# Optimization experiments

Measured on AMD Instinct MI355X. Metric: run time of the kernel, lower is better.

## Reference

```python
import jax, jax.numpy as jnp
import numpy as np

B, T, D, E, K = 4, 4096, 2048, 64, 2


def setup_inputs() -> dict:
    key = jax.random.key(0)
    k1, k2 = jax.random.split(key)
    x = jax.random.normal(k1, (B, T, D), dtype=jnp.float32)
    # nn.Linear(token_dim, n_experts, bias=False) weight: [E, D]
    gate_w = jax.random.normal(k2, (E, D), dtype=jnp.float32) * (1.0 / np.sqrt(D))
    return {"x": x, "gate_w": gate_w}


def reference(x, gate_w):
    # logits = x @ gate_w.T : [B, T, E]
    logits = jnp.einsum("btd,ed->bte", x, gate_w)
    scores, indices = jax.lax.top_k(logits, K)  # [B, T, K] each
    weights = jax.nn.softmax(scores, axis=-1)
    return weights, indices
```

## Files before the change

### kernel.cpp

```cpp
#include <hip/hip_runtime.h>
#include <math.h>


#define NTOK 16384
#define DDIM 2048
#define NEXP 64
#define TBLK 64
#define KC   32
#define NKG  4
#define NCH  16

typedef __attribute__((ext_vector_type(8))) _Float16 f16x8;
typedef __attribute__((ext_vector_type(4))) float f32x4;

#define XF_OFF 0
#define WF_OFF 98304

__device__ static inline void gload_lds16(const void* gsrc, void* ldst) {
    __builtin_amdgcn_global_load_lds(
        (const __attribute__((address_space(1))) void*)gsrc,
        (__attribute__((address_space(3))) void*)ldst, 16, 0, 0);
}

__device__ static inline void split2h(float x, _Float16& h, _Float16& m) {
    h = (_Float16)x;
    float r = x - (float)h;
    m = (_Float16)r;
}

__global__ __launch_bounds__(512, 1) void moe_fused_kernel(
    const float* __restrict__ x,
    const float* __restrict__ gw,
    float* __restrict__ out)
{
    extern __shared__ char smem[];
    float4* XF = (float4*)(smem + XF_OFF);
    float4* WF = (float4*)(smem + WF_OFF);
    float*  red = (float*)smem;

    const int tid  = threadIdx.x;
    const int lane = tid & 63;
    const int w    = tid >> 6;
    const int kg   = w >> 1;
    const int tq   = w & 1;
    const int T0   = blockIdx.x * TBLK;

    const int fr  = lane & 15;
    const int fg  = lane >> 4;
    const int akey = fr & 7;

    f32x4 acc[2][4];
#pragma unroll
    for (int mi = 0; mi < 2; ++mi)
#pragma unroll
        for (int n = 0; n < 4; ++n) acc[mi][n] = (f32x4){0.f, 0.f, 0.f, 0.f};

#define XSTAGE(ch, buf)                                                       \
    {                                                                         \
        _Pragma("unroll")                                                     \
        for (int k = 0; k < 4; ++k) {                                         \
            const int u = tid + k * 512;                                      \
            const int s = u >> 9;                                             \
            const int r = (u >> 3) & 63;                                      \
            const int c = (u & 7) ^ (r & 7);                                  \
            gload_lds16(x + (size_t)(T0 + r) * DDIM + ((ch) * NKG + s) * KC + c * 4, \
                        &XF[(buf) * 2048 + u]);                               \
        }                                                                     \
    }
#define WSTAGE(ch, buf)                                                       \
    {                                                                         \
        _Pragma("unroll")                                                     \
        for (int k = 0; k < 4; ++k) {                                         \
            const int u = tid + k * 512;                                      \
            const int s = u >> 9;                                             \
            const int e = (u >> 3) & 63;                                      \
            const int c = (u & 7) ^ (e & 7);                                  \
            gload_lds16(gw + (size_t)e * DDIM + ((ch) * NKG + s) * KC + c * 4,\
                        &WF[(buf) * 2048 + u]);                               \
        }                                                                     \
    }
#define WAIT4 asm volatile("s_waitcnt vmcnt(4)" ::: "memory")
#define WAIT0 asm volatile("s_waitcnt vmcnt(0)" ::: "memory")
#define BAR   __builtin_amdgcn_s_barrier()

    XSTAGE(0, 0); WSTAGE(0, 0); XSTAGE(1, 1);
    WAIT4; BAR;

    for (int ch = 0; ch < NCH; ++ch) {
        const int xb = ch % 3;
        const int wb = ch & 1;
        if (ch + 1 < NCH) WSTAGE(ch + 1, (ch + 1) & 1);
        if (ch + 2 < NCH) XSTAGE(ch + 2, (ch + 2) % 3);

        const float4* Xc = &XF[xb * 2048 + kg * 512];
        f16x8 ah[2], am[2];
#pragma unroll
        for (int mi = 0; mi < 2; ++mi) {
            const int arow = (tq * 32 + mi * 16 + fr) * 8;
            float4 a0 = Xc[arow + ((fg * 2 + 0) ^ akey)];
            float4 a1 = Xc[arow + ((fg * 2 + 1) ^ akey)];
            float xf8[8] = {a0.x, a0.y, a0.z, a0.w, a1.x, a1.y, a1.z, a1.w};
#pragma unroll
            for (int j = 0; j < 8; ++j) {
                _Float16 hj, mj;
                split2h(xf8[j], hj, mj);
                ah[mi][j] = hj; am[mi][j] = mj;
            }
        }

        const float4* Wc = &WF[wb * 2048 + kg * 512];
#pragma unroll
        for (int n = 0; n < 4; ++n) {
            const int brow = (n * 16 + fr) * 8;
            float4 b0 = Wc[brow + ((fg * 2 + 0) ^ akey)];
            float4 b1 = Wc[brow + ((fg * 2 + 1) ^ akey)];
            float wf8[8] = {b0.x, b0.y, b0.z, b0.w, b1.x, b1.y, b1.z, b1.w};
            f16x8 bh, bm;
#pragma unroll
            for (int j = 0; j < 8; ++j) {
                _Float16 hj, mj;
                split2h(wf8[j], hj, mj);
                bh[j] = hj; bm[j] = mj;
            }
#pragma unroll
            for (int mi = 0; mi < 2; ++mi) {
                acc[mi][n] = __builtin_amdgcn_mfma_f32_16x16x32_f16(am[mi], bm, acc[mi][n], 0, 0, 0);
                acc[mi][n] = __builtin_amdgcn_mfma_f32_16x16x32_f16(am[mi], bh, acc[mi][n], 0, 0, 0);
                acc[mi][n] = __builtin_amdgcn_mfma_f32_16x16x32_f16(ah[mi], bm, acc[mi][n], 0, 0, 0);
                acc[mi][n] = __builtin_amdgcn_mfma_f32_16x16x32_f16(ah[mi], bh, acc[mi][n], 0, 0, 0);
            }
        }

        if (ch + 2 < NCH)      { WAIT4; BAR; }
        else if (ch + 1 < NCH) { WAIT0; BAR; }
        else                   { BAR; }
    }
#undef XSTAGE
#undef WSTAGE
#undef WAIT4
#undef WAIT0
#undef BAR

#pragma unroll
    for (int mi = 0; mi < 2; ++mi)
#pragma unroll
        for (int n = 0; n < 4; ++n)
#pragma unroll
            for (int j = 0; j < 4; ++j) {
                const int e = n * 16 + fr;
                const int t = tq * 32 + mi * 16 + fg * 4 + j;
                red[kg * 4160 + e * 65 + t] = acc[mi][n][j];
            }
    __syncthreads();

#pragma unroll
    for (int k = 0; k < 8; ++k) {
        const int q = tid + k * 512;
        const int e = q >> 6;
        const int t = q & 63;
        float s = red[0 * 4160 + e * 65 + t];
#pragma unroll
        for (int sl = 1; sl < NKG; ++sl)
            s += red[sl * 4160 + e * 65 + t];
        red[e * 65 + t] = s;
    }
    __syncthreads();

    if (tid < TBLK) {
        const int t = tid;
        float m1 = -INFINITY, m2 = -INFINITY;
        int i1 = 0, i2 = 0;
        for (int e = 0; e < NEXP; ++e) {
            float v = red[e * 65 + t];
            if (v > m1) {
                m2 = m1; i2 = i1;
                m1 = v;  i1 = e;
            } else if (v > m2) {
                m2 = v;  i2 = e;
            }
        }
        float e2 = expf(m2 - m1);
        float denom = 1.f + e2;
        const int gt = T0 + t;
        out[gt * 2 + 0] = 1.f / denom;
        out[gt * 2 + 1] = e2 / denom;
        out[NTOK * 2 + gt * 2 + 0] = (float)i1;
        out[NTOK * 2 + gt * 2 + 1] = (float)i2;
    }
}

extern "C" void kernel_launch(void* const* d_in, const int* in_sizes, int n_in,
                              void* d_out, int out_size, void* d_ws, size_t ws_size,
                              hipStream_t stream) {
    const float* x  = (const float*)d_in[0];
    const float* gw = (const float*)d_in[1];
    float* out = (float*)d_out;
    (void)d_ws; (void)ws_size;

    moe_fused_kernel<<<dim3(NTOK / TBLK), dim3(512), 163840, stream>>>(
        x, gw, out);
}
```

Baseline: 41.29 us.

## Shrink token tile to 32 with 256-thread blocks for two blocks per CU

Halves the token tile per block (64 to 32), halves the K-split groups and thread count, and cuts LDS per block so two blocks can fit per CU. The grid doubles to 512 blocks, which improves wave coverage across CUs and lets one block's loads overlap another's compute. The cost is that the gate weight matrix is streamed from L2 twice as often per token, and each block has less MFMA work between barriers.

```diff
diff --git a/kernel.cpp b/kernel.cpp
--- a/kernel.cpp
+++ b/kernel.cpp
@@ -5,16 +5,16 @@
 #define NTOK 16384
 #define DDIM 2048
 #define NEXP 64
-#define TBLK 64
+#define TBLK 32
 #define KC   32
-#define NKG  4
-#define NCH  16
+#define NKG  2
+#define NCH  32
 
 typedef __attribute__((ext_vector_type(8))) _Float16 f16x8;
 typedef __attribute__((ext_vector_type(4))) float f32x4;
 
 #define XF_OFF 0
-#define WF_OFF 98304
+#define WF_OFF 24576
 
 __device__ static inline void gload_lds16(const void* gsrc, void* ldst) {
     __builtin_amdgcn_global_load_lds(
@@ -28,7 +28,7 @@
     m = (_Float16)r;
 }
 
-__global__ __launch_bounds__(512, 1) void moe_fused_kernel(
+__global__ __launch_bounds__(256, 2) void moe_fused_kernel(
     const float* __restrict__ x,
     const float* __restrict__ gw,
     float* __restrict__ out)
@@ -49,42 +49,40 @@
     const int fg  = lane >> 4;
     const int akey = fr & 7;
 
-    f32x4 acc[2][4];
+    f32x4 acc[4];
 #pragma unroll
-    for (int mi = 0; mi < 2; ++mi)
-#pragma unroll
-        for (int n = 0; n < 4; ++n) acc[mi][n] = (f32x4){0.f, 0.f, 0.f, 0.f};
+    for (int n = 0; n < 4; ++n) acc[n] = (f32x4){0.f, 0.f, 0.f, 0.f};
 
 #define XSTAGE(ch, buf)                                                       \
     {                                                                         \
         _Pragma("unroll")                                                     \
-        for (int k = 0; k < 4; ++k) {                                         \
-            const int u = tid + k * 512;                                      \
-            const int s = u >> 9;                                             \
-            const int r = (u >> 3) & 63;                                      \
+        for (int k = 0; k < 2; ++k) {                                         \
+            const int u = tid + k * 256;                                      \
+            const int s = u >> 8;                                             \
+            const int r = (u >> 3) & 31;                                      \
             const int c = (u & 7) ^ (r & 7);                                  \
             gload_lds16(x + (size_t)(T0 + r) * DDIM + ((ch) * NKG + s) * KC + c * 4, \
-                        &XF[(buf) * 2048 + u]);                               \
+                        &XF[(buf) * 512 + u]);                                \
         }                                                                     \
     }
 #define WSTAGE(ch, buf)                                                       \
     {                                                                         \
         _Pragma("unroll")                                                     \
         for (int k = 0; k < 4; ++k) {                                         \
-            const int u = tid + k * 512;                                      \
+            const int u = tid + k * 256;                                      \
             const int s = u >> 9;                                             \
             const int e = (u >> 3) & 63;                                      \
             const int c = (u & 7) ^ (e & 7);                                  \
             gload_lds16(gw + (size_t)e * DDIM + ((ch) * NKG + s) * KC + c * 4,\
-                        &WF[(buf) * 2048 + u]);                               \
+                        &WF[(buf) * 1024 + u]);                               \
         }                                                                     \
     }
-#define WAIT4 asm volatile("s_waitcnt vmcnt(4)" ::: "memory")
+#define WAIT2 asm volatile("s_waitcnt vmcnt(2)" ::: "memory")
 #define WAIT0 asm volatile("s_waitcnt vmcnt(0)" ::: "memory")
 #define BAR   __builtin_amdgcn_s_barrier()
 
     XSTAGE(0, 0); WSTAGE(0, 0); XSTAGE(1, 1);
-    WAIT4; BAR;
+    WAIT2; BAR;
 
     for (int ch = 0; ch < NCH; ++ch) {
         const int xb = ch % 3;
@@ -92,11 +90,10 @@
         if (ch + 1 < NCH) WSTAGE(ch + 1, (ch + 1) & 1);
         if (ch + 2 < NCH) XSTAGE(ch + 2, (ch + 2) % 3);
 
-        const float4* Xc = &XF[xb * 2048 + kg * 512];
-        f16x8 ah[2], am[2];
-#pragma unroll
-        for (int mi = 0; mi < 2; ++mi) {
-            const int arow = (tq * 32 + mi * 16 + fr) * 8;
+        const float4* Xc = &XF[xb * 512 + kg * 256];
+        f16x8 ah, am;
+        {
+            const int arow = (tq * 16 + fr) * 8;
             float4 a0 = Xc[arow + ((fg * 2 + 0) ^ akey)];
             float4 a1 = Xc[arow + ((fg * 2 + 1) ^ akey)];
             float xf8[8] = {a0.x, a0.y, a0.z, a0.w, a1.x, a1.y, a1.z, a1.w};
@@ -104,11 +101,11 @@
             for (int j = 0; j < 8; ++j) {
                 _Float16 hj, mj;
                 split2h(xf8[j], hj, mj);
-                ah[mi][j] = hj; am[mi][j] = mj;
+                ah[j] = hj; am[j] = mj;
             }
         }
 
-        const float4* Wc = &WF[wb * 2048 + kg * 512];
+        const float4* Wc = &WF[wb * 1024 + kg * 512];
 #pragma unroll
         for (int n = 0; n < 4; ++n) {
             const int brow = (n * 16 + fr) * 8;
@@ -122,47 +119,38 @@
                 split2h(wf8[j], hj, mj);
                 bh[j] = hj; bm[j] = mj;
             }
-#pragma unroll
-            for (int mi = 0; mi < 2; ++mi) {
-                acc[mi][n] = __builtin_amdgcn_mfma_f32_16x16x32_f16(am[mi], bm, acc[mi][n], 0, 0, 0);
-                acc[mi][n] = __builtin_amdgcn_mfma_f32_16x16x32_f16(am[mi], bh, acc[mi][n], 0, 0, 0);
-                acc[mi][n] = __builtin_amdgcn_mfma_f32_16x16x32_f16(ah[mi], bm, acc[mi][n], 0, 0, 0);
-                acc[mi][n] = __builtin_amdgcn_mfma_f32_16x16x32_f16(ah[mi], bh, acc[mi][n], 0, 0, 0);
-            }
+            acc[n] = __builtin_amdgcn_mfma_f32_16x16x32_f16(am, bm, acc[n], 0, 0, 0);
+            acc[n] = __builtin_amdgcn_mfma_f32_16x16x32_f16(am, bh, acc[n], 0, 0, 0);
+            acc[n] = __builtin_amdgcn_mfma_f32_16x16x32_f16(ah, bm, acc[n], 0, 0, 0);
+            acc[n] = __builtin_amdgcn_mfma_f32_16x16x32_f16(ah, bh, acc[n], 0, 0, 0);
         }
 
-        if (ch + 2 < NCH)      { WAIT4; BAR; }
+        if (ch + 2 < NCH)      { WAIT2; BAR; }
         else if (ch + 1 < NCH) { WAIT0; BAR; }
         else                   { BAR; }
     }
 #undef XSTAGE
 #undef WSTAGE
-#undef WAIT4
+#undef WAIT2
 #undef WAIT0
 #undef BAR
 
 #pragma unroll
-    for (int mi = 0; mi < 2; ++mi)
+    for (int n = 0; n < 4; ++n)
 #pragma unroll
-        for (int n = 0; n < 4; ++n)
-#pragma unroll
-            for (int j = 0; j < 4; ++j) {
-                const int e = n * 16 + fr;
-                const int t = tq * 32 + mi * 16 + fg * 4 + j;
-                red[kg * 4160 + e * 65 + t] = acc[mi][n][j];
-            }
+        for (int j = 0; j < 4; ++j) {
+            const int e = n * 16 + fr;
+            const int t = tq * 16 + fg * 4 + j;
+            red[kg * 2112 + e * 33 + t] = acc[n][j];
+        }
     __syncthreads();
 
 #pragma unroll
     for (int k = 0; k < 8; ++k) {
-        const int q = tid + k * 512;
-        const int e = q >> 6;
-        const int t = q & 63;
-        float s = red[0 * 4160 + e * 65 + t];
-#pragma unroll
-        for (int sl = 1; sl < NKG; ++sl)
-            s += red[sl * 4160 + e * 65 + t];
-        red[e * 65 + t] = s;
+        const int q = tid + k * 256;
+        const int e = q >> 5;
+        const int t = q & 31;
+        red[e * 33 + t] = red[e * 33 + t] + red[2112 + e * 33 + t];
     }
     __syncthreads();
 
@@ -171,7 +159,7 @@
         float m1 = -INFINITY, m2 = -INFINITY;
         int i1 = 0, i2 = 0;
         for (int e = 0; e < NEXP; ++e) {
-            float v = red[e * 65 + t];
+            float v = red[e * 33 + t];
             if (v > m1) {
                 m2 = m1; i2 = i1;
                 m1 = v;  i1 = e;
@@ -197,6 +185,6 @@
     float* out = (float*)d_out;
     (void)d_ws; (void)ws_size;
 
-    moe_fused_kernel<<<dim3(NTOK / TBLK), dim3(512), 163840, stream>>>(
+    moe_fused_kernel<<<dim3(NTOK / TBLK), dim3(256), 57344, stream>>>(
         x, gw, out);
 }
```

Result: slower. 49.95 us (+21.0%).
